# Kernel optimization log

Measured on AMD Instinct MI355X. Metric: run time of the kernel, lower is better.

## Reference

```python
import jax, jax.numpy as jnp
import numpy as np

V, A, L = 10000, 600, 6          # dx vocab, num ancestors, ancestors-per-leaf
O, E = 128, 128                  # ontoEmbDim, EHREmbDim
ATD, PTD, DPL = 128, 128, 500    # ontoattnDim, ptattnDim, dpLabelSize
B, T, N = 64, 32, 40             # batch, visits, codes-per-visit


def _l2norm(x):
    return x / jnp.maximum(jnp.linalg.norm(x, axis=-1, keepdims=True), 1e-12)


def setup_inputs() -> dict:
    key = jax.random.key(0)
    ks = jax.random.split(key, 16)
    g = lambda k, shape, fan: (jax.random.normal(k, shape) / np.sqrt(fan)).astype(jnp.float32)
    dxseqs = jax.random.randint(ks[0], (B, T, N), 0, V + 1)          # V = padding idx
    dx_onehot = jax.random.uniform(ks[1], (T, B, V), dtype=jnp.float32)
    leaves = jax.random.randint(ks[2], (V, L), 0, V)
    ancestors = jax.random.randint(ks[3], (V, L), V, V + A)
    ehr_table = g(ks[4], (V + 1, E), E).at[V].set(0.0)               # padding row zero
    return dict(
        dxseqs=dxseqs, dx_onehot=dx_onehot, leaves=leaves, ancestors=ancestors,
        onto_table=g(ks[5], (V + A, O), O),
        onto_Wa=g(ks[6], (2 * O, ATD), 2 * O), onto_ba=jnp.zeros((ATD,), jnp.float32),
        onto_Wc=g(ks[7], (ATD, 1), ATD), onto_bc=jnp.zeros((1,), jnp.float32),
        ehr_table=ehr_table,
        attn_W=g(ks[8], (2 * E + 2 * O, PTD), 2 * E + 2 * O), attn_b=jnp.zeros((PTD,), jnp.float32),
        comb_W=g(ks[9], (PTD, 1), PTD), comb_b=jnp.zeros((1,), jnp.float32),
        co_W=g(ks[10], (E, V), E), co_b=jnp.zeros((V,), jnp.float32),
        dp_W=g(ks[11], (O + E, DPL), O + E), dp_b=jnp.zeros((DPL,), jnp.float32),
    )


def _forward(dxseqs, dx_onehot, leaves, ancestors, onto_table, onto_Wa, onto_ba,
             onto_Wc, onto_bc, ehr_table, attn_W, attn_b, comb_W, comb_b,
             co_W, co_b, dp_W, dp_b):
    # --- OntoEmb (GRAM-style ancestor attention) ---
    el = onto_table[leaves]                                  # (V, L, O)
    ea = onto_table[ancestors]                               # (V, L, O)
    h = jnp.tanh(jnp.concatenate([el, ea], -1) @ onto_Wa + onto_ba)
    a = jax.nn.softmax(h @ onto_Wc + onto_bc, axis=1)        # (V, L, 1)
    onto_all = jnp.concatenate(
        [jnp.sum(a * ea, axis=1), jnp.zeros((1, O), onto_table.dtype)], axis=0)  # (V+1, O)

    dxOnto = onto_all[dxseqs]                                # (B, T, N, O)
    ontoV = jnp.einsum('tbv,vo->bto', dx_onehot, onto_all[:-1])  # (B, T, O)
    dxEHR = ehr_table[dxseqs]                                # (B, T, N, E)
    ehrV = _l2norm(jnp.sum(dxEHR, axis=2))                   # (B, T, E)

    # --- cooccurrence branch ---
    cooccurU = jax.nn.softmax(ehrV @ co_W + co_b, axis=2)    # (B, T, V)
    vonehot = jnp.transpose(dx_onehot, (1, 0, 2))            # (B, T, V)
    cooccur_loss = -jnp.mean(jnp.sum(vonehot * jnp.log(cooccurU), axis=(1, 2)))

    # --- additive (Bahdanau) attention over codes in a visit ---
    dxEmb = jnp.concatenate([dxEHR, dxOnto], -1)             # (B, T, N, E+O)
    vs = jnp.concatenate([ontoV, ehrV], -1)[:, :, None, :]   # (B, T, 1, O+E)
    attnInput = jnp.concatenate([jnp.broadcast_to(vs, dxEmb.shape), dxEmb], -1)
    mlp = jnp.tanh(attnInput @ attn_W + attn_b)              # (B, T, N, PTD)
    attn = jax.nn.softmax(mlp @ comb_W + comb_b, axis=2)     # (B, T, N, 1)
    vs2 = jnp.sum(attn * dxEmb, axis=2)                      # (B, T, E+O)

    dp = jax.nn.softmax(jnp.tanh(_l2norm(vs2)) @ dp_W + dp_b, axis=2)  # (B, T, DPL)
    return dp, cooccur_loss * 10.0


def reference(dxseqs, dx_onehot, leaves, ancestors, onto_table, onto_Wa, onto_ba,
              onto_Wc, onto_bc, ehr_table, attn_W, attn_b, comb_W, comb_b,
              co_W, co_b, dp_W, dp_b):
    return _forward(dxseqs, dx_onehot, leaves, ancestors, onto_table, onto_Wa, onto_ba,
                    onto_Wc, onto_bc, ehr_table, attn_W, attn_b, comb_W, comb_b,
                    co_W, co_b, dp_W, dp_b)
```

## Files before the change

kernel.cpp:

```cpp
#include <hip/hip_runtime.h>
#include <math.h>

typedef float4 f4;
typedef __bf16 bf16x8 __attribute__((ext_vector_type(8)));
typedef float f32x4 __attribute__((ext_vector_type(4)));

static constexpr int kV = 10000, kL = 6, kDPL = 500;
static constexpr int kB = 64, kT = 32, kN = 40, kBT = 2048;
static constexpr int kXC = 5;
static constexpr int kNB = 272;
static constexpr int kLd = 10240;
static constexpr int kNP = 313;
static constexpr int kVT2 = 40;

#define MFMA16 __builtin_amdgcn_mfma_f32_16x16x32_bf16

__device__ __forceinline__ bf16x8 cvt8(f4 a, f4 b) {
  bf16x8 r;
  r[0] = (__bf16)a.x; r[1] = (__bf16)a.y; r[2] = (__bf16)a.z; r[3] = (__bf16)a.w;
  r[4] = (__bf16)b.x; r[5] = (__bf16)b.y; r[6] = (__bf16)b.z; r[7] = (__bf16)b.w;
  return r;
}

__global__ __launch_bounds__(256) void mmore_cvt_bf16(
    const float* __restrict__ in, __bf16* __restrict__ out, int n) {
  int i = (blockIdx.x * 256 + threadIdx.x) * 8;
  if (i < n) {
    f4 a = *(const f4*)(in + i), b = *(const f4*)(in + i + 4);
    *(bf16x8*)(out + i) = cvt8(a, b);
  }
}

__global__ __launch_bounds__(256) void mmore_trcvt(
    const float* __restrict__ in, __bf16* __restrict__ out,
    int K, int N, int Kpad) {
  int t = threadIdx.x;
  int n = blockIdx.y * 16 + (t & 15);
  int kb = (blockIdx.x * 16 + (t >> 4)) * 8;
  bf16x8 r;
  #pragma unroll
  for (int i = 0; i < 8; ++i) {
    int k = kb + i;
    float v = (k < K && n < N) ? in[(size_t)k * N + n] : 0.f;
    r[i] = (__bf16)v;
  }
  *(bf16x8*)(out + (size_t)n * Kpad + kb) = r;
}

__global__ __launch_bounds__(256) void mmore_brow(
    const float* __restrict__ coW, const float* __restrict__ cob,
    __bf16* __restrict__ Btab) {
  int id = blockIdx.x * 256 + threadIdx.x;
  int rr = id / 1280;
  int kk = (id - rr * 1280) * 8;
  bf16x8 r;
  #pragma unroll
  for (int i = 0; i < 8; ++i) {
    int k = kk + i;
    float v = 0.f;
    if (k < kV) {
      if (rr < 128) v = coW[(size_t)rr * kV + k];
      else if (rr == 128) v = cob[k];
      else if (rr == 129) v = 1.f;
    }
    r[i] = (__bf16)v;
  }
  *(bf16x8*)(Btab + (size_t)(128 + rr) * kLd + kk) = r;
}

__global__ __launch_bounds__(256) void mmore_panelize(
    const __bf16* __restrict__ Btab, __bf16* __restrict__ Bp) {
  int t = threadIdx.x;
  int S = blockIdx.x, ry = blockIdx.y;
  int row = ry * 16 + (t >> 4), kk = (t & 15) * 2;
  unsigned v = *(const unsigned*)(Btab + (size_t)row * kLd + S * 32 + kk);
  *(unsigned*)(Bp + ((size_t)S * kNB + row) * 32 + kk) = v;
}

__global__ __launch_bounds__(128) void mmore_ehrv(
    const int* __restrict__ dxseqs, const float* __restrict__ ehr_table,
    float* __restrict__ ehrV) {
  int bt = blockIdx.x, t = threadIdx.x;
  const int* row = dxseqs + bt * kN;
  float acc = 0.f;
  for (int n = 0; n < kN; ++n) acc += ehr_table[(size_t)row[n] * 128 + t];
  float v = acc * acc;
  #pragma unroll
  for (int off = 32; off; off >>= 1) v += __shfl_down(v, off);
  __shared__ float red[2];
  if ((t & 63) == 0) red[t >> 6] = v;
  __syncthreads();
  float ss = red[0] + red[1];
  float inv = 1.f / fmaxf(sqrtf(ss), 1e-12f);
  ehrV[bt * 128 + t] = acc * inv;
}

__global__ __launch_bounds__(256) void mmore_scores_mfma(
    const __bf16* __restrict__ otb, const int* __restrict__ leaves,
    const int* __restrict__ anc, const __bf16* __restrict__ WaT,
    const float* __restrict__ ba, const float* __restrict__ Wc,
    const float* __restrict__ bc, float* __restrict__ s_out) {
  int t = threadIdx.x, wave = t >> 6, lane = t & 63, lm = lane & 15, lg = lane >> 4;
  int r0 = blockIdx.x * 32;
  int rA0 = r0 + lm, rA1 = rA0 + 16;
  int v0 = rA0 / 6, l0 = rA0 - v0 * 6, v1 = rA1 / 6, l1 = rA1 - v1 * 6;
  const __bf16* pL0 = otb + (size_t)leaves[v0 * 6 + l0] * 128;
  const __bf16* pA0 = otb + (size_t)anc[v0 * 6 + l0] * 128;
  const __bf16* pL1 = otb + (size_t)leaves[v1 * 6 + l1] * 128;
  const __bf16* pA1 = otb + (size_t)anc[v1 * 6 + l1] * 128;
  const __bf16* bp = WaT + (size_t)(wave * 32 + lm) * 256 + lg * 8;
  f32x4 acc[2][2] = {};
  #pragma unroll
  for (int kb = 0; kb < 256; kb += 32) {
    int k = kb + lg * 8;
    const __bf16* s0 = (k < 128) ? (pL0 + k) : (pA0 + (k - 128));
    const __bf16* s1 = (k < 128) ? (pL1 + k) : (pA1 + (k - 128));
    bf16x8 a0 = *(const bf16x8*)s0;
    bf16x8 a1 = *(const bf16x8*)s1;
    bf16x8 b0 = *(const bf16x8*)(bp + kb);
    bf16x8 b1 = *(const bf16x8*)(bp + kb + 16 * 256);
    acc[0][0] = MFMA16(a0, b0, acc[0][0], 0, 0, 0);
    acc[0][1] = MFMA16(a0, b1, acc[0][1], 0, 0, 0);
    acc[1][0] = MFMA16(a1, b0, acc[1][0], 0, 0, 0);
    acc[1][1] = MFMA16(a1, b1, acc[1][1], 0, 0, 0);
  }
  __shared__ float red[4][32];
  float bcv = bc[0];
  #pragma unroll
  for (int mf = 0; mf < 2; ++mf) {
    #pragma unroll
    for (int j = 0; j < 4; ++j) {
      float p = 0.f;
      #pragma unroll
      for (int nf = 0; nf < 2; ++nf) {
        int c = wave * 32 + nf * 16 + lm;
        p += tanhf(acc[mf][nf][j] + ba[c]) * Wc[c];
      }
      #pragma unroll
      for (int off = 8; off; off >>= 1) p += __shfl_xor(p, off);
      if (lm == 0) red[wave][mf * 16 + lg * 4 + j] = p;
    }
  }
  __syncthreads();
  if (t < 32) s_out[r0 + t] = red[0][t] + red[1][t] + red[2][t] + red[3][t] + bcv;
}

__global__ __launch_bounds__(128) void mmore_onto(
    const float* __restrict__ ot, const int* __restrict__ anc,
    const float* __restrict__ s_in, float* __restrict__ onto_all) {
  int v = blockIdx.x, t = threadIdx.x;
  if (v == kV) { onto_all[(size_t)v * 128 + t] = 0.f; return; }
  __shared__ float sv[kL];
  __shared__ int aidx[kL];
  if (t < kL) { sv[t] = s_in[v * kL + t]; aidx[t] = anc[v * kL + t]; }
  __syncthreads();
  float mx = sv[0];
  #pragma unroll
  for (int l = 1; l < kL; ++l) mx = fmaxf(mx, sv[l]);
  float e[kL], sum = 0.f;
  #pragma unroll
  for (int l = 0; l < kL; ++l) { e[l] = expf(sv[l] - mx); sum += e[l]; }
  float acc = 0.f;
  #pragma unroll
  for (int l = 0; l < kL; ++l)
    acc += (e[l] / sum) * ot[(size_t)aidx[l] * 128 + t];
  onto_all[(size_t)v * 128 + t] = acc;
}

__global__ __launch_bounds__(256) void mmore_xgemm(
    const float* __restrict__ X, const __bf16* __restrict__ Bp,
    float* __restrict__ part) {
  int t = threadIdx.x, w = t >> 6, lane = t & 63, lm = lane & 15, lg = lane >> 4;
  int bid = blockIdx.x;
  int swz = (bid & 7) * 80 + (bid >> 3);
  int btile = swz & 127, chunk = swz >> 7;
  int r0 = btile * 16;
  bool lastc = (chunk == kXC - 1);
  int nsteps = lastc ? 56 : 64;
  int f0 = w * 4;
  const float* ap = X + (size_t)(r0 + lm) * kV + chunk * 2048 + lg * 8;
  const __bf16* bp = Bp + ((size_t)(chunk * 64) * kNB + lm) * 32 + lg * 8;
  f32x4 acc[5] = {};
  #pragma unroll 4
  for (int s = 0; s < nsteps; ++s) {
    f4 x0 = *(const f4*)(ap + s * 32);
    f4 x1 = *(const f4*)(ap + s * 32 + 4);
    bf16x8 af = cvt8(x0, x1);
    const __bf16* bs = bp + (size_t)s * (kNB * 32);
    acc[0] = MFMA16(af, *(const bf16x8*)(bs + (f0 + 0) * 512), acc[0], 0, 0, 0);
    acc[1] = MFMA16(af, *(const bf16x8*)(bs + (f0 + 1) * 512), acc[1], 0, 0, 0);
    acc[2] = MFMA16(af, *(const bf16x8*)(bs + (f0 + 2) * 512), acc[2], 0, 0, 0);
    acc[3] = MFMA16(af, *(const bf16x8*)(bs + (f0 + 3) * 512), acc[3], 0, 0, 0);
    if (w == 3)
      acc[4] = MFMA16(af, *(const bf16x8*)(bs + 16 * 512), acc[4], 0, 0, 0);
  }
  if (lastc) {
    f4 z = make_float4(0.f, 0.f, 0.f, 0.f), x0 = z, x1 = z;
    if (lg < 2) {
      x0 = *(const f4*)(ap + 56 * 32);
      x1 = *(const f4*)(ap + 56 * 32 + 4);
    }
    bf16x8 af = cvt8(x0, x1);
    const __bf16* bs = bp + (size_t)56 * (kNB * 32);
    acc[0] = MFMA16(af, *(const bf16x8*)(bs + (f0 + 0) * 512), acc[0], 0, 0, 0);
    acc[1] = MFMA16(af, *(const bf16x8*)(bs + (f0 + 1) * 512), acc[1], 0, 0, 0);
    acc[2] = MFMA16(af, *(const bf16x8*)(bs + (f0 + 2) * 512), acc[2], 0, 0, 0);
    acc[3] = MFMA16(af, *(const bf16x8*)(bs + (f0 + 3) * 512), acc[3], 0, 0, 0);
    if (w == 3)
      acc[4] = MFMA16(af, *(const bf16x8*)(bs + 16 * 512), acc[4], 0, 0, 0);
  }
  #pragma unroll
  for (int j = 0; j < 4; ++j) {
    int r = r0 + lg * 4 + j;
    int bt = (r & 63) * kT + (r >> 6);
    size_t o = ((size_t)chunk * kBT + bt) * kNB;
    #pragma unroll
    for (int f = 0; f < 4; ++f) part[o + (f0 + f) * 16 + lm] = acc[f][j];
    if (w == 3) part[o + 256 + lm] = acc[4][j];
  }
}

__global__ __launch_bounds__(256) void mmore_creduce(
    const float* __restrict__ part, float* __restrict__ ontoV,
    float* __restrict__ pwred, float* __restrict__ pc, float* __restrict__ sp) {
  int bt = blockIdx.x, t = threadIdx.x;
  for (int c = t; c < kNB; c += 256) {
    float a = 0.f;
    #pragma unroll
    for (int ch = 0; ch < kXC; ++ch)
      a += part[((size_t)ch * kBT + bt) * kNB + c];
    if (c < 128) ontoV[(size_t)bt * 128 + c] = a;
    else if (c < 256) pwred[(size_t)bt * 128 + (c - 128)] = a;
    else if (c == 256) pc[bt] = a;
    else if (c == 257) sp[bt] = a;
  }
}

__global__ __launch_bounds__(256) void mmore_lossg(
    const float* __restrict__ ehrV, const __bf16* __restrict__ coWT,
    const float* __restrict__ cob, float* __restrict__ epart) {
  int t = threadIdx.x, wave = t >> 6, lane = t & 63, lm = lane & 15, lg = lane >> 4;
  int vt = blockIdx.x, btile = blockIdx.y;
  int r0 = btile * 32, vb = vt * 256;
  const float* a0 = ehrV + (size_t)(r0 + lm) * 128 + lg * 8;
  const float* a1 = a0 + 16 * 128;
  f32x4 acc[2][4] = {};
  #pragma unroll
  for (int kb = 0; kb < 128; kb += 32) {
    f4 x0 = *(const f4*)(a0 + kb), x1 = *(const f4*)(a0 + kb + 4);
    f4 y0 = *(const f4*)(a1 + kb), y1 = *(const f4*)(a1 + kb + 4);
    bf16x8 af0 = cvt8(x0, x1), af1 = cvt8(y0, y1);
    #pragma unroll
    for (int nf = 0; nf < 4; ++nf) {
      int c = vb + wave * 64 + nf * 16 + lm;
      bf16x8 b = *(const bf16x8*)(coWT + (size_t)c * 128 + kb + lg * 8);
      acc[0][nf] = MFMA16(af0, b, acc[0][nf], 0, 0, 0);
      acc[1][nf] = MFMA16(af1, b, acc[1][nf], 0, 0, 0);
    }
  }
  float se[2][4] = {};
  #pragma unroll
  for (int nf = 0; nf < 4; ++nf) {
    int c = vb + wave * 64 + nf * 16 + lm;
    if (c < kV) {
      float cb = cob[c];
      #pragma unroll
      for (int mf = 0; mf < 2; ++mf)
        #pragma unroll
        for (int j = 0; j < 4; ++j)
          se[mf][j] += __expf(acc[mf][nf][j] + cb);
    }
  }
  __shared__ float red[4][32];
  #pragma unroll
  for (int mf = 0; mf < 2; ++mf)
    #pragma unroll
    for (int j = 0; j < 4; ++j) {
      float v = se[mf][j];
      #pragma unroll
      for (int off = 8; off; off >>= 1) v += __shfl_xor(v, off);
      if (lm == 0) red[wave][mf * 16 + lg * 4 + j] = v;
    }
  __syncthreads();
  if (t < 32)
    epart[(size_t)vt * kBT + r0 + t] =
        red[0][t] + red[1][t] + red[2][t] + red[3][t];
}

__global__ __launch_bounds__(256) void mmore_lossterm(
    const float* __restrict__ ehrV, const float* __restrict__ pwred,
    const float* __restrict__ pc, const float* __restrict__ sp,
    const float* __restrict__ epart, float* __restrict__ term) {
  int t = threadIdx.x;
  int bt = blockIdx.x * 16 + (t >> 4);
  int sub = t & 15;
  const f4* e = (const f4*)(ehrV + (size_t)bt * 128 + sub * 8);
  const f4* w = (const f4*)(pwred + (size_t)bt * 128 + sub * 8);
  f4 e0 = e[0], e1 = e[1], w0 = w[0], w1 = w[1];
  float d = e0.x * w0.x + e0.y * w0.y + e0.z * w0.z + e0.w * w0.w +
            e1.x * w1.x + e1.y * w1.y + e1.z * w1.z + e1.w * w1.w;
  float S = 0.f;
  for (int vt = sub; vt < kVT2; vt += 16) S += epart[(size_t)vt * kBT + bt];
  #pragma unroll
  for (int off = 8; off; off >>= 1) {
    d += __shfl_xor(d, off); S += __shfl_xor(S, off);
  }
  if (sub == 0) term[bt] = (d + pc[bt]) - sp[bt] * logf(S);
}

__global__ __launch_bounds__(256) void mmore_lossfin(
    const float* __restrict__ term, float* __restrict__ out) {
  int t = threadIdx.x;
  float a = 0.f;
  for (int i = t; i < kBT; i += 256) a += term[i];
  #pragma unroll
  for (int off = 32; off; off >>= 1) a += __shfl_down(a, off);
  __shared__ float red[4];
  if ((t & 63) == 0) red[t >> 6] = a;
  __syncthreads();
  if (t == 0) out[0] = -(10.f / 64.f) * (red[0] + red[1] + red[2] + red[3]);
}

__global__ __launch_bounds__(256) void mmore_gemm_mfma(
    const float* __restrict__ A, const __bf16* __restrict__ WT,
    int ldWT, int koff, const float* __restrict__ bias,
    float* __restrict__ C, int M, int accumulate) {
  int t = threadIdx.x, wave = t >> 6, lane = t & 63, lm = lane & 15, lg = lane >> 4;
  int r0 = blockIdx.x * 32;
  int row0 = r0 + lm, row1 = row0 + 16;
  bool ok0 = row0 < M, ok1 = row1 < M;
  const float* a0 = A + (size_t)row0 * 128 + lg * 8;
  const float* a1 = A + (size_t)row1 * 128 + lg * 8;
  const __bf16* bp = WT + (size_t)(wave * 32 + lm) * ldWT + koff + lg * 8;
  int ld16 = 16 * ldWT;
  f32x4 acc[2][2] = {};
  #pragma unroll
  for (int kb = 0; kb < 128; kb += 32) {
    f4 x0 = make_float4(0, 0, 0, 0), x1 = x0, y0 = x0, y1 = x0;
    if (ok0) { x0 = *(const f4*)(a0 + kb); x1 = *(const f4*)(a0 + kb + 4); }
    if (ok1) { y0 = *(const f4*)(a1 + kb); y1 = *(const f4*)(a1 + kb + 4); }
    bf16x8 af0 = cvt8(x0, x1), af1 = cvt8(y0, y1);
    bf16x8 b0 = *(const bf16x8*)(bp + kb);
    bf16x8 b1 = *(const bf16x8*)(bp + kb + ld16);
    acc[0][0] = MFMA16(af0, b0, acc[0][0], 0, 0, 0);
    acc[0][1] = MFMA16(af0, b1, acc[0][1], 0, 0, 0);
    acc[1][0] = MFMA16(af1, b0, acc[1][0], 0, 0, 0);
    acc[1][1] = MFMA16(af1, b1, acc[1][1], 0, 0, 0);
  }
  #pragma unroll
  for (int mf = 0; mf < 2; ++mf)
    #pragma unroll
    for (int nf = 0; nf < 2; ++nf) {
      int col = wave * 32 + nf * 16 + lm;
      #pragma unroll
      for (int j = 0; j < 4; ++j) {
        int row = r0 + mf * 16 + lg * 4 + j;
        if (row < M) {
          float v = acc[mf][nf][j];
          if (bias) v += bias[col];
          if (accumulate) v += C[(size_t)row * 128 + col];
          C[(size_t)row * 128 + col] = v;
        }
      }
    }
}

__device__ __forceinline__ float mmore_block_sum(float v, float* red) {
  int t = threadIdx.x;
  #pragma unroll
  for (int off = 32; off; off >>= 1) v += __shfl_down(v, off);
  if ((t & 63) == 0) red[t >> 6] = v;
  __syncthreads();
  if (t == 0) red[0] = red[0] + red[1] + red[2] + red[3];
  __syncthreads();
  return red[0];
}

__global__ __launch_bounds__(256) void mmore_attn(
    const int* __restrict__ dxseqs, const float* __restrict__ base,
    const float* __restrict__ pe, const float* __restrict__ po,
    const float* __restrict__ combW, const float* __restrict__ combB,
    const float* __restrict__ ehr_table, const float* __restrict__ onto_all,
    float* __restrict__ tn) {
  __shared__ float base_s[128];
  __shared__ int idx_s[kN];
  __shared__ float scp[kN][2];
  __shared__ float attn_s[64];
  __shared__ float red[4];
  int bt = blockIdx.x, t = threadIdx.x;
  if (t < 128) base_s[t] = base[bt * 128 + t];
  if (t < kN) idx_s[t] = dxseqs[bt * kN + t];
  __syncthreads();
  int c = t & 127, half = t >> 7, wid = t >> 6, lane = t & 63;
  float cw = combW[c];
  for (int n2 = 0; n2 < kN / 2; ++n2) {
    int n = n2 * 2 + half;
    int id = idx_s[n];
    float x = base_s[c] + pe[(size_t)id * 128 + c] + po[(size_t)id * 128 + c];
    float val = tanhf(x) * cw;
    #pragma unroll
    for (int off = 32; off; off >>= 1) val += __shfl_down(val, off);
    if (lane == 0) scp[n][wid & 1] = val;
  }
  __syncthreads();
  if (t < 64) {
    float s = (t < kN) ? (scp[t][0] + scp[t][1] + combB[0]) : -1e30f;
    float mx = s;
    #pragma unroll
    for (int off = 32; off; off >>= 1) mx = fmaxf(mx, __shfl_xor(mx, off));
    float e = (t < kN) ? __expf(s - mx) : 0.f;
    float sm = e;
    #pragma unroll
    for (int off = 32; off; off >>= 1) sm += __shfl_xor(sm, off);
    attn_s[t] = e / sm;
  }
  __syncthreads();
  float acc = 0.f;
  {
    const float* tab = (t < 128) ? ehr_table : onto_all;
    int j = t & 127;
    for (int n = 0; n < kN; ++n)
      acc += attn_s[n] * tab[(size_t)idx_s[n] * 128 + j];
  }
  float ss = mmore_block_sum(acc * acc, red);
  float inv = 1.f / fmaxf(sqrtf(ss), 1e-12f);
  tn[(size_t)bt * 256 + t] = tanhf(acc * inv);
}

__global__ __launch_bounds__(256) void mmore_dpgemm(
    const float* __restrict__ tn, const __bf16* __restrict__ dpWT,
    const float* __restrict__ dpB, float* __restrict__ u) {
  int t = threadIdx.x, wave = t >> 6, lane = t & 63, lm = lane & 15, lg = lane >> 4;
  int c0 = blockIdx.x * 128, r0 = blockIdx.y * 32;
  const float* a0 = tn + (size_t)(r0 + lm) * 256 + lg * 8;
  const float* a1 = a0 + 16 * 256;
  const __bf16* bp = dpWT + (size_t)(c0 + wave * 32 + lm) * 256 + lg * 8;
  f32x4 acc[2][2] = {};
  #pragma unroll
  for (int kb = 0; kb < 256; kb += 32) {
    f4 x0 = *(const f4*)(a0 + kb), x1 = *(const f4*)(a0 + kb + 4);
    f4 y0 = *(const f4*)(a1 + kb), y1 = *(const f4*)(a1 + kb + 4);
    bf16x8 af0 = cvt8(x0, x1), af1 = cvt8(y0, y1);
    bf16x8 b0 = *(const bf16x8*)(bp + kb);
    bf16x8 b1 = *(const bf16x8*)(bp + kb + 16 * 256);
    acc[0][0] = MFMA16(af0, b0, acc[0][0], 0, 0, 0);
    acc[0][1] = MFMA16(af0, b1, acc[0][1], 0, 0, 0);
    acc[1][0] = MFMA16(af1, b0, acc[1][0], 0, 0, 0);
    acc[1][1] = MFMA16(af1, b1, acc[1][1], 0, 0, 0);
  }
  #pragma unroll
  for (int mf = 0; mf < 2; ++mf)
    #pragma unroll
    for (int nf = 0; nf < 2; ++nf) {
      int col = c0 + wave * 32 + nf * 16 + lm;
      float bias = (col < kDPL) ? dpB[col] : 0.f;
      #pragma unroll
      for (int j = 0; j < 4; ++j) {
        int row = r0 + mf * 16 + lg * 4 + j;
        u[(size_t)row * 512 + col] = acc[mf][nf][j] + bias;
      }
    }
}

__global__ __launch_bounds__(128) void mmore_dpsoft(
    const float* __restrict__ u, float* __restrict__ out) {
  int bt = blockIdx.x, t = threadIdx.x;
  __shared__ float red[2];
  float v[4]; float mx = -1e30f;
  #pragma unroll
  for (int i = 0; i < 4; ++i) {
    int c = t + i * 128;
    v[i] = (c < kDPL) ? u[(size_t)bt * 512 + c] : -1e30f;
    mx = fmaxf(mx, v[i]);
  }
  #pragma unroll
  for (int off = 32; off; off >>= 1) mx = fmaxf(mx, __shfl_xor(mx, off));
  if ((t & 63) == 0) red[t >> 6] = mx;
  __syncthreads();
  mx = fmaxf(red[0], red[1]);
  __syncthreads();
  float e[4], s = 0.f;
  #pragma unroll
  for (int i = 0; i < 4; ++i) {
    int c = t + i * 128;
    e[i] = (c < kDPL) ? __expf(v[i] - mx) : 0.f;
    s += e[i];
  }
  #pragma unroll
  for (int off = 32; off; off >>= 1) s += __shfl_xor(s, off);
  if ((t & 63) == 0) red[t >> 6] = s;
  __syncthreads();
  float invS = 1.f / (red[0] + red[1]);
  #pragma unroll
  for (int i = 0; i < 4; ++i) {
    int c = t + i * 128;
    if (c < kDPL) out[(size_t)bt * kDPL + c] = e[i] * invS;
  }
}

extern "C" void kernel_launch(void* const* d_in, const int* in_sizes, int n_in,
                              void* d_out, int out_size, void* d_ws, size_t ws_size,
                              hipStream_t stream) {
  const int*   dxseqs     = (const int*)d_in[0];
  const float* dx_onehot  = (const float*)d_in[1];
  const int*   leaves     = (const int*)d_in[2];
  const int*   ancestors  = (const int*)d_in[3];
  const float* onto_table = (const float*)d_in[4];
  const float* onto_Wa    = (const float*)d_in[5];
  const float* onto_ba    = (const float*)d_in[6];
  const float* onto_Wc    = (const float*)d_in[7];
  const float* onto_bc    = (const float*)d_in[8];
  const float* ehr_table  = (const float*)d_in[9];
  const float* attn_W     = (const float*)d_in[10];
  const float* attn_b     = (const float*)d_in[11];
  const float* comb_W     = (const float*)d_in[12];
  const float* comb_b     = (const float*)d_in[13];
  const float* co_W       = (const float*)d_in[14];
  const float* co_b       = (const float*)d_in[15];
  const float* dp_W       = (const float*)d_in[16];
  const float* dp_b       = (const float*)d_in[17];
  float* out = (float*)d_out;

  float* ws = (float*)d_ws;
  size_t off = 0;
  auto alloc = [&](size_t n) { float* p = ws + off; off += n; return p; };
  float* onto_all = alloc((size_t)(kV + 1) * 128);
  float* s_sc     = alloc((size_t)kV * kL);
  float* ehrV     = alloc((size_t)kBT * 128);
  float* ontoV    = alloc((size_t)kBT * 128);
  __bf16* Bp      = (__bf16*)alloc((size_t)kNP * kNB * 32 / 2);
  __bf16* attn_WT = (__bf16*)alloc((size_t)128 * 512 / 2);
  __bf16* dpWT    = (__bf16*)alloc((size_t)512 * 256 / 2);
  __bf16* WaT     = (__bf16*)alloc((size_t)128 * 256 / 2);
  float* peR      = alloc((size_t)(kV + 1) * 128);
  float* poR      = alloc((size_t)(kV + 1) * 128);
  float* basep    = alloc((size_t)kBT * 128);
  float* epart    = alloc((size_t)kVT2 * kBT);
  float* pwred    = alloc((size_t)kBT * 128);
  float* pc       = alloc(kBT);
  float* sp       = alloc(kBT);
  float* term     = alloc(kBT);
  __bf16* ot_bf = (__bf16*)peR;
  __bf16* BtabL = (__bf16*)peR;
  float*  cpart = peR;
  __bf16* coWT  = (__bf16*)peR;
  float*  u     = peR;
  float*  tn    = ehrV;

  mmore_cvt_bf16<<<663, 256, 0, stream>>>(onto_table, ot_bf, 10600 * 128);
  mmore_trcvt<<<dim3(2, 8), 256, 0, stream>>>(onto_Wa, WaT, 256, 128, 256);
  mmore_trcvt<<<dim3(4, 8), 256, 0, stream>>>(attn_W, attn_WT, 512, 128, 512);
  mmore_trcvt<<<dim3(2, 32), 256, 0, stream>>>(dp_W, dpWT, 256, kDPL, 256);

  mmore_ehrv<<<kBT, 128, 0, stream>>>(dxseqs, ehr_table, ehrV);
  mmore_scores_mfma<<<(kV * kL) / 32, 256, 0, stream>>>(
      ot_bf, leaves, ancestors, WaT, onto_ba, onto_Wc, onto_bc, s_sc);
  mmore_onto<<<kV + 1, 128, 0, stream>>>(onto_table, ancestors, s_sc, onto_all);
  mmore_trcvt<<<dim3(80, 8), 256, 0, stream>>>(onto_all, BtabL, kV, 128, kLd);
  mmore_brow<<<720, 256, 0, stream>>>(co_W, co_b, BtabL);
  mmore_panelize<<<dim3(kNP, 17), 256, 0, stream>>>(BtabL, Bp);
  mmore_xgemm<<<128 * kXC, 256, 0, stream>>>(dx_onehot, Bp, cpart);
  mmore_creduce<<<kBT, 256, 0, stream>>>(cpart, ontoV, pwred, pc, sp);
  mmore_trcvt<<<dim3(1, 640), 256, 0, stream>>>(co_W, coWT, 128, kV, 128);
  mmore_lossg<<<dim3(kVT2, 64), 256, 0, stream>>>(ehrV, coWT, co_b, epart);
  mmore_lossterm<<<kBT / 16, 256, 0, stream>>>(ehrV, pwred, pc, sp, epart, term);
  mmore_lossfin<<<1, 256, 0, stream>>>(term, out + (size_t)kBT * kDPL);
  mmore_gemm_mfma<<<313, 256, 0, stream>>>(ehr_table, attn_WT, 512, 256, nullptr, peR, kV + 1, 0);
  mmore_gemm_mfma<<<313, 256, 0, stream>>>(onto_all, attn_WT, 512, 384, nullptr, poR, kV + 1, 0);
  mmore_gemm_mfma<<<64, 256, 0, stream>>>(ontoV, attn_WT, 512, 0, nullptr, basep, kBT, 0);
  mmore_gemm_mfma<<<64, 256, 0, stream>>>(ehrV, attn_WT, 512, 128, attn_b, basep, kBT, 1);
  mmore_attn<<<kBT, 256, 0, stream>>>(dxseqs, basep, peR, poR, comb_W, comb_b,
                                      ehr_table, onto_all, tn);
  mmore_dpgemm<<<dim3(4, 64), 256, 0, stream>>>(tn, dpWT, dp_b, u);
  mmore_dpsoft<<<kBT, 128, 0, stream>>>(u, out);
}
```

Measured before the change: 304.6 us.

## Double-buffer X tiles in LDS via async global_load_lds in xgemm

The xgemm kernel now stages the fp32 X activation tile (16 rows by 256 columns) into double-buffered LDS using direct global-to-LDS loads with an XOR swizzle. The next stage is prefetched while MFMAs consume the current one, replacing per-lane strided global loads. The aim is to hide global memory latency behind compute and get better coalesced row loads. In exchange it adds LDS use, a barrier per stage and a full vmcnt(0) wait that also blocks on the B-operand loads.

```diff
diff --git a/kernel.cpp b/kernel.cpp
--- a/kernel.cpp
+++ b/kernel.cpp
@@ -14,6 +14,12 @@
 static constexpr int kVT2 = 40;
 
 #define MFMA16 __builtin_amdgcn_mfma_f32_16x16x32_bf16
+
+typedef const __attribute__((address_space(1))) unsigned int ga_u32;
+typedef __attribute__((address_space(3))) unsigned int lds_u32;
+__device__ __forceinline__ void gll16(const float* g, float* l) {
+  __builtin_amdgcn_global_load_lds((ga_u32*)g, (lds_u32*)l, 16, 0, 0);
+}
 
 __device__ __forceinline__ bf16x8 cvt8(f4 a, f4 b) {
   bf16x8 r;
@@ -170,23 +176,65 @@
 __global__ __launch_bounds__(256) void mmore_xgemm(
     const float* __restrict__ X, const __bf16* __restrict__ Bp,
     float* __restrict__ part) {
+  __shared__ __align__(16) float Xs[2][16][256];
   int t = threadIdx.x, w = t >> 6, lane = t & 63, lm = lane & 15, lg = lane >> 4;
   int bid = blockIdx.x;
   int swz = (bid & 7) * 80 + (bid >> 3);
   int btile = swz & 127, chunk = swz >> 7;
   int r0 = btile * 16;
   bool lastc = (chunk == kXC - 1);
-  int nsteps = lastc ? 56 : 64;
+  int nSS = lastc ? 7 : 8;
+  int kbase = chunk * 2048;
   int f0 = w * 4;
-  const float* ap = X + (size_t)(r0 + lm) * kV + chunk * 2048 + lg * 8;
   const __bf16* bp = Bp + ((size_t)(chunk * 64) * kNB + lm) * 32 + lg * 8;
   f32x4 acc[5] = {};
-  #pragma unroll 4
-  for (int s = 0; s < nsteps; ++s) {
-    f4 x0 = *(const f4*)(ap + s * 32);
-    f4 x1 = *(const f4*)(ap + s * 32 + 4);
+
+#define XGV6_STAGE(db, S)                                                     \
+  {                                                                           \
+    _Pragma("unroll")                                                         \
+    for (int u = 0; u < 4; ++u) {                                             \
+      int row_ = w * 4 + u;                                                   \
+      const float* src_ = X + (size_t)(r0 + row_) * kV + kbase + (S) * 256 +  \
+                          ((lane ^ (row_ & 7)) << 2);                         \
+      gll16(src_, &Xs[db][row_][0]);                                          \
+    }                                                                         \
+  }
+
+  XGV6_STAGE(0, 0);
+  asm volatile("s_waitcnt vmcnt(0)" ::: "memory");
+  __builtin_amdgcn_s_barrier();
+  int buf = 0;
+  for (int S = 0; S < nSS; ++S) {
+    if (S + 1 < nSS) {
+      if (buf == 0) { XGV6_STAGE(1, S + 1); } else { XGV6_STAGE(0, S + 1); }
+    }
+    #pragma unroll
+    for (int j = 0; j < 8; ++j) {
+      int G0 = 8 * j + 2 * lg;
+      int sw0 = G0 ^ (lm & 7), sw1 = (G0 + 1) ^ (lm & 7);
+      f4 x0 = *(const f4*)&Xs[buf][lm][sw0 * 4];
+      f4 x1 = *(const f4*)&Xs[buf][lm][sw1 * 4];
+      bf16x8 af = cvt8(x0, x1);
+      const __bf16* bs = bp + (size_t)(S * 8 + j) * (kNB * 32);
+      acc[0] = MFMA16(af, *(const bf16x8*)(bs + (f0 + 0) * 512), acc[0], 0, 0, 0);
+      acc[1] = MFMA16(af, *(const bf16x8*)(bs + (f0 + 1) * 512), acc[1], 0, 0, 0);
+      acc[2] = MFMA16(af, *(const bf16x8*)(bs + (f0 + 2) * 512), acc[2], 0, 0, 0);
+      acc[3] = MFMA16(af, *(const bf16x8*)(bs + (f0 + 3) * 512), acc[3], 0, 0, 0);
+      if (w == 3)
+        acc[4] = MFMA16(af, *(const bf16x8*)(bs + 16 * 512), acc[4], 0, 0, 0);
+    }
+    asm volatile("s_waitcnt vmcnt(0)" ::: "memory");
+    __builtin_amdgcn_s_barrier();
+    buf ^= 1;
+  }
+  if (lastc) {
+    f4 z = make_float4(0.f, 0.f, 0.f, 0.f), x0 = z, x1 = z;
+    if (lg < 2) {
+      const float* xp = X + (size_t)(r0 + lm) * kV + 9984 + lg * 8;
+      x0 = *(const f4*)xp; x1 = *(const f4*)(xp + 4);
+    }
     bf16x8 af = cvt8(x0, x1);
-    const __bf16* bs = bp + (size_t)s * (kNB * 32);
+    const __bf16* bs = Bp + ((size_t)312 * kNB + lm) * 32 + lg * 8;
     acc[0] = MFMA16(af, *(const bf16x8*)(bs + (f0 + 0) * 512), acc[0], 0, 0, 0);
     acc[1] = MFMA16(af, *(const bf16x8*)(bs + (f0 + 1) * 512), acc[1], 0, 0, 0);
     acc[2] = MFMA16(af, *(const bf16x8*)(bs + (f0 + 2) * 512), acc[2], 0, 0, 0);
@@ -194,21 +242,6 @@
     if (w == 3)
       acc[4] = MFMA16(af, *(const bf16x8*)(bs + 16 * 512), acc[4], 0, 0, 0);
   }
-  if (lastc) {
-    f4 z = make_float4(0.f, 0.f, 0.f, 0.f), x0 = z, x1 = z;
-    if (lg < 2) {
-      x0 = *(const f4*)(ap + 56 * 32);
-      x1 = *(const f4*)(ap + 56 * 32 + 4);
-    }
-    bf16x8 af = cvt8(x0, x1);
-    const __bf16* bs = bp + (size_t)56 * (kNB * 32);
-    acc[0] = MFMA16(af, *(const bf16x8*)(bs + (f0 + 0) * 512), acc[0], 0, 0, 0);
-    acc[1] = MFMA16(af, *(const bf16x8*)(bs + (f0 + 1) * 512), acc[1], 0, 0, 0);
-    acc[2] = MFMA16(af, *(const bf16x8*)(bs + (f0 + 2) * 512), acc[2], 0, 0, 0);
-    acc[3] = MFMA16(af, *(const bf16x8*)(bs + (f0 + 3) * 512), acc[3], 0, 0, 0);
-    if (w == 3)
-      acc[4] = MFMA16(af, *(const bf16x8*)(bs + 16 * 512), acc[4], 0, 0, 0);
-  }
   #pragma unroll
   for (int j = 0; j < 4; ++j) {
     int r = r0 + lg * 4 + j;
@@ -218,6 +251,7 @@
     for (int f = 0; f < 4; ++f) part[o + (f0 + f) * 16 + lm] = acc[f][j];
     if (w == 3) part[o + 256 + lm] = acc[4][j];
   }
+#undef XGV6_STAGE
 }
 
 __global__ __launch_bounds__(256) void mmore_creduce(
```

Result: faster. 287.5 us (-5.6%).
